# Kernel optimization log

Hardware: AMD Instinct MI355X
Metric: run time of the kernel (lower is better)

## Reference

```python
import jax, jax.numpy as jnp
import numpy as np

AH, AW, TD = 7, 7, 4
SPATIAL_SCALE = 0.0625
TEMP_SCALE = 1.0


def setup_inputs() -> dict:
    key = jax.random.key(0)
    ks = jax.random.split(key, 8)
    N, C, T, H, W = 2, 256, 16, 64, 64
    R = 1024
    features = jax.random.normal(ks[0], (N, C, T, H, W), dtype=jnp.float32)
    img = W / SPATIAL_SCALE  # 1024 px original image
    b = jax.random.randint(ks[1], (R,), 0, N).astype(jnp.float32)
    x1 = jax.random.uniform(ks[2], (R,), minval=0.0, maxval=img * 0.7)
    y1 = jax.random.uniform(ks[3], (R,), minval=0.0, maxval=img * 0.7)
    x2 = x1 + jax.random.uniform(ks[4], (R,), minval=32.0, maxval=img * 0.3)
    y2 = y1 + jax.random.uniform(ks[5], (R,), minval=32.0, maxval=img * 0.3)
    t1 = jax.random.uniform(ks[6], (R,), minval=0.0, maxval=(T - 1) * 0.5)
    t2 = t1 + jax.random.uniform(ks[7], (R,), minval=1.0, maxval=(T - 1) * 0.5)
    rois = jnp.stack([b, x1, y1, t1, x2, y2, t2], axis=1)  # [R,7]
    return {"features": features, "rois": rois}


def _axis_samples(start, end, n, size):
    # legacy roi_align: n grid points spanning the roi, bin = extent/(n-1)
    bin_sz = jnp.maximum(end - start, 0.0) / (n - 1)
    c = start[:, None] + bin_sz[:, None] * jnp.arange(n, dtype=start.dtype)  # [R,n]
    lo = jnp.clip(jnp.floor(c), 0, size - 2).astype(jnp.int32)
    return lo, c - lo, (c >= 0) & (c < size)


def _roi_align_avg(features, rois):
    N, C, T, H, W = features.shape
    Tg, Hg, Wg = TD + 1, AH + 1, AW + 1  # sample on a +1 grid, then avg-pool back
    b = rois[:, 0].astype(jnp.int32)
    t0, ft, vt = _axis_samples(rois[:, 3] * TEMP_SCALE, rois[:, 6] * TEMP_SCALE, Tg, T)
    h0, fh, vh = _axis_samples(rois[:, 2] * SPATIAL_SCALE, rois[:, 5] * SPATIAL_SCALE, Hg, H)
    w0, fw, vw = _axis_samples(rois[:, 1] * SPATIAL_SCALE, rois[:, 4] * SPATIAL_SCALE, Wg, W)
    fm = jnp.transpose(features, (0, 2, 3, 4, 1))  # [N,T,H,W,C] channel-last gather
    b4 = b[:, None, None, None]
    R = rois.shape[0]
    out = jnp.zeros((R, Tg, Hg, Wg, C), dtype=features.dtype)
    for dt in (0, 1):  # 8-corner trilinear interpolation
        wt = ft if dt else (1.0 - ft)
        for dh in (0, 1):
            wh = fh if dh else (1.0 - fh)
            for dw in (0, 1):
                ww = fw if dw else (1.0 - fw)
                corner = fm[b4,
                            (t0 + dt)[:, :, None, None],
                            (h0 + dh)[:, None, :, None],
                            (w0 + dw)[:, None, None, :]]  # [R,Tg,Hg,Wg,C]
                w8 = wt[:, :, None, None] * wh[:, None, :, None] * ww[:, None, None, :]
                out = out + w8[..., None] * corner
    valid = vt[:, :, None, None] & vh[:, None, :, None] & vw[:, None, None, :]
    out = out * valid[..., None].astype(out.dtype)  # samples outside feature map -> 0

    def pool_pairs(a, axis):
        # adaptive_avg_pool from K+1 -> K == kernel-2 stride-1 average
        n = a.shape[axis]
        return 0.5 * (jax.lax.slice_in_dim(a, 0, n - 1, axis=axis)
                      + jax.lax.slice_in_dim(a, 1, n, axis=axis))

    out = pool_pairs(pool_pairs(pool_pairs(out, 1), 2), 3)  # [R,TD,AH,AW,C]
    return jnp.transpose(out, (0, 4, 1, 2, 3))  # [R,C,TD,AH,AW]


def reference(features, rois):
    return _roi_align_avg(features, rois)
```

## Files before the change

### kernel.cpp

```cpp
#include <hip/hip_runtime.h>

#define C_CH 256
#define T_SZ 16
#define H_SZ 64
#define W_SZ 64
#define TGN 5
#define CH 8
#define HWs (H_SZ * W_SZ)
#define CSTR (T_SZ * HWs)
#define NOUT 196
#define KMAX 10

__device__ __forceinline__ float2 ld2a(const float* p) {
    const float2* q = (const float2*)__builtin_assume_aligned(p, 8);
    return *q;
}

__global__ __launch_bounds__(256, 8) void roialign3d_kernel(
    const float* __restrict__ features,
    const float* __restrict__ rois,
    float* __restrict__ out)
{
    const int bid   = blockIdx.x;
    const int sr    = bid >> 13;
    const int rem   = bid & 8191;
    const int r     = rem >> 3;
    const int chunk = (sr << 3) | (rem & 7);
    const int c0    = chunk * CH;

    const int tid  = threadIdx.x;
    const int lane = tid & 63;
    const int wid  = __builtin_amdgcn_readfirstlane(tid >> 6);
    const int hg   = lane >> 3;
    const int wg   = lane & 7;

    __shared__ __align__(16) float sB[KMAX][4];
    __shared__ int sU0, sK;

    const float* roi = rois + r * 7;
    const int   b   = __builtin_amdgcn_readfirstlane((int)roi[0]);
    const float rx1 = roi[1], ry1 = roi[2];
    const float rx2 = roi[4], ry2 = roi[5];

    if (tid < KMAX) {
        const float rt1 = roi[3], rt2 = roi[6];
        const float tbin = fmaxf(rt2 - rt1, 0.0f) * 0.25f;
        int t0a[TGN]; float tw0a[TGN], tw1a[TGN];
        #pragma unroll
        for (int i = 0; i < TGN; ++i) {
            float c  = rt1 + tbin * (float)i;
            float lo = fminf(fmaxf(floorf(c), 0.0f), 14.0f);
            float f  = c - lo;
            float v  = (c >= 0.0f && c < 16.0f) ? 0.125f : 0.0f;
            t0a[i]  = (int)lo;
            tw0a[i] = v * (1.0f - f);
            tw1a[i] = v * f;
        }
        const int u0 = t0a[0];
        const int s0 = u0 + tid;
        float av[TGN];
        #pragma unroll
        for (int i = 0; i < TGN; ++i)
            av[i] = (t0a[i] == s0 ? tw0a[i] : 0.0f)
                  + (t0a[i] + 1 == s0 ? tw1a[i] : 0.0f);
        sB[tid][0] = av[0] + av[1];
        sB[tid][1] = av[1] + av[2];
        sB[tid][2] = av[2] + av[3];
        sB[tid][3] = av[3] + av[4];
        if (tid == 0) { sU0 = u0; sK = t0a[TGN - 1] + 2 - u0; }
    }

    const float hs = ry1 * 0.0625f, he = ry2 * 0.0625f;
    const float hbin = fmaxf(he - hs, 0.0f) * (1.0f / 7.0f);
    const float hc  = hs + hbin * (float)hg;
    const float hlo = fminf(fmaxf(floorf(hc), 0.0f), 62.0f);
    const float hf  = hc - hlo;
    const float hv  = (hc >= 0.0f && hc < 64.0f) ? 1.0f : 0.0f;
    const int   h0  = (int)hlo;
    const float hw0 = hv * (1.0f - hf), hw1 = hv * hf;

    const float wss = rx1 * 0.0625f, wee = rx2 * 0.0625f;
    const float wbin = fmaxf(wee - wss, 0.0f) * (1.0f / 7.0f);
    const float wc  = wss + wbin * (float)wg;
    const float wlo = fminf(fmaxf(floorf(wc), 0.0f), 62.0f);
    const float wf  = wc - wlo;
    const float wv  = (wc >= 0.0f && wc < 64.0f) ? 1.0f : 0.0f;
    const int   w0  = (int)wlo;
    const float ww0 = wv * (1.0f - wf), ww1 = wv * wf;

    const float w00 = hw0 * ww0, w01 = hw0 * ww1;
    const float w10 = hw1 * ww0, w11 = hw1 * ww1;
    const int hw_off = h0 * W_SZ + w0;

    __syncthreads();
    const int u0   = __builtin_amdgcn_readfirstlane(sU0);
    const int kcnt = __builtin_amdgcn_readfirstlane(sK);

    const bool active = (hg < 7) && (wg < 7);
    const int  s_hw   = hg * 7 + wg;

    const float* fcA = features
        + ((size_t)b * C_CH + (size_t)(c0 + wid * 2)) * CSTR
        + (size_t)u0 * HWs + hw_off;
    const float* fcB = fcA + CSTR;

    float oA[4] = {0.f, 0.f, 0.f, 0.f};
    float oB[4] = {0.f, 0.f, 0.f, 0.f};

    #pragma unroll
    for (int u = 0; u < KMAX; ++u) {
        if (u < 2 || u < kcnt) {
            const float4 bb = *(const float4*)sB[u];
            const float* pA = fcA + u * HWs;
            const float* pB = fcB + u * HWs;
            float2 rA0 = ld2a(pA);
            float2 rA1 = ld2a(pA + W_SZ);
            float2 rB0 = ld2a(pB);
            float2 rB1 = ld2a(pB + W_SZ);

            const float bilA = rA0.x * w00 + rA0.y * w01 + rA1.x * w10 + rA1.y * w11;
            const float bilB = rB0.x * w00 + rB0.y * w01 + rB1.x * w10 + rB1.y * w11;

            oA[0] += bb.x * bilA; oA[1] += bb.y * bilA;
            oA[2] += bb.z * bilA; oA[3] += bb.w * bilA;
            oB[0] += bb.x * bilB; oB[1] += bb.y * bilB;
            oB[2] += bb.z * bilB; oB[3] += bb.w * bilB;
        }
    }

    float* ob = out + ((size_t)r * C_CH + (size_t)(c0 + wid * 2)) * NOUT;
    #pragma unroll
    for (int td = 0; td < 4; ++td) {
        float o = oA[td];
        o += __shfl_down(o, 1);
        o += __shfl_down(o, 8);
        if (active) __builtin_nontemporal_store(o, &ob[td * 49 + s_hw]);
    }
    ob += NOUT;
    #pragma unroll
    for (int td = 0; td < 4; ++td) {
        float o = oB[td];
        o += __shfl_down(o, 1);
        o += __shfl_down(o, 8);
        if (active) __builtin_nontemporal_store(o, &ob[td * 49 + s_hw]);
    }
}

extern "C" void kernel_launch(void* const* d_in, const int* in_sizes, int n_in,
                              void* d_out, int out_size, void* d_ws, size_t ws_size,
                              hipStream_t stream) {
    const float* features = (const float*)d_in[0];
    const float* rois     = (const float*)d_in[1];
    float* out            = (float*)d_out;

    int R = in_sizes[1] / 7;
    int nblocks = R * (C_CH / CH);
    hipLaunchKernelGGL(roialign3d_kernel, dim3(nblocks), dim3(256), 0, stream,
                       features, rois, out);
}
```

Measured before the change: 129.7 us.

## Add fast path loading float4 row segments covering two width samples per lane

When the ROI's width bin is at most two pixels, each lane now loads one 4-wide row segment from each of two rows. That segment covers both corners of two adjacent width samples, and each wave handles two channels by splitting lanes into halves. The aim is to halve the number of global load instructions, since the narrow bins let neighbouring samples share the same cache lines. Wider ROIs fall back to the original path. This adds a wave-uniform branch, more select logic for per-position weights, and a reshuffled reduction. The float4 loads assume 16-byte alignment that the computed offsets do not guarantee.

```diff
diff --git a/kernel.cpp b/kernel.cpp
--- a/kernel.cpp
+++ b/kernel.cpp
@@ -13,6 +13,10 @@
 
 __device__ __forceinline__ float2 ld2a(const float* p) {
     const float2* q = (const float2*)__builtin_assume_aligned(p, 8);
+    return *q;
+}
+__device__ __forceinline__ float4 ld4a(const float* p) {
+    const float4* q = (const float4*)__builtin_assume_aligned(p, 16);
     return *q;
 }
 
@@ -31,8 +35,6 @@
     const int tid  = threadIdx.x;
     const int lane = tid & 63;
     const int wid  = __builtin_amdgcn_readfirstlane(tid >> 6);
-    const int hg   = lane >> 3;
-    const int wg   = lane & 7;
 
     __shared__ __align__(16) float sB[KMAX][4];
     __shared__ int sU0, sK;
@@ -69,80 +71,166 @@
         sB[tid][3] = av[3] + av[4];
         if (tid == 0) { sU0 = u0; sK = t0a[TGN - 1] + 2 - u0; }
     }
-
-    const float hs = ry1 * 0.0625f, he = ry2 * 0.0625f;
-    const float hbin = fmaxf(he - hs, 0.0f) * (1.0f / 7.0f);
-    const float hc  = hs + hbin * (float)hg;
-    const float hlo = fminf(fmaxf(floorf(hc), 0.0f), 62.0f);
-    const float hf  = hc - hlo;
-    const float hv  = (hc >= 0.0f && hc < 64.0f) ? 1.0f : 0.0f;
-    const int   h0  = (int)hlo;
-    const float hw0 = hv * (1.0f - hf), hw1 = hv * hf;
-
-    const float wss = rx1 * 0.0625f, wee = rx2 * 0.0625f;
-    const float wbin = fmaxf(wee - wss, 0.0f) * (1.0f / 7.0f);
-    const float wc  = wss + wbin * (float)wg;
-    const float wlo = fminf(fmaxf(floorf(wc), 0.0f), 62.0f);
-    const float wf  = wc - wlo;
-    const float wv  = (wc >= 0.0f && wc < 64.0f) ? 1.0f : 0.0f;
-    const int   w0  = (int)wlo;
-    const float ww0 = wv * (1.0f - wf), ww1 = wv * wf;
-
-    const float w00 = hw0 * ww0, w01 = hw0 * ww1;
-    const float w10 = hw1 * ww0, w11 = hw1 * ww1;
-    const int hw_off = h0 * W_SZ + w0;
-
     __syncthreads();
     const int u0   = __builtin_amdgcn_readfirstlane(sU0);
     const int kcnt = __builtin_amdgcn_readfirstlane(sK);
 
-    const bool active = (hg < 7) && (wg < 7);
-    const int  s_hw   = hg * 7 + wg;
-
-    const float* fcA = features
-        + ((size_t)b * C_CH + (size_t)(c0 + wid * 2)) * CSTR
-        + (size_t)u0 * HWs + hw_off;
-    const float* fcB = fcA + CSTR;
-
-    float oA[4] = {0.f, 0.f, 0.f, 0.f};
-    float oB[4] = {0.f, 0.f, 0.f, 0.f};
-
-    #pragma unroll
-    for (int u = 0; u < KMAX; ++u) {
-        if (u < 2 || u < kcnt) {
-            const float4 bb = *(const float4*)sB[u];
-            const float* pA = fcA + u * HWs;
-            const float* pB = fcB + u * HWs;
-            float2 rA0 = ld2a(pA);
-            float2 rA1 = ld2a(pA + W_SZ);
-            float2 rB0 = ld2a(pB);
-            float2 rB1 = ld2a(pB + W_SZ);
-
-            const float bilA = rA0.x * w00 + rA0.y * w01 + rA1.x * w10 + rA1.y * w11;
-            const float bilB = rB0.x * w00 + rB0.y * w01 + rB1.x * w10 + rB1.y * w11;
-
-            oA[0] += bb.x * bilA; oA[1] += bb.y * bilA;
-            oA[2] += bb.z * bilA; oA[3] += bb.w * bilA;
-            oB[0] += bb.x * bilB; oB[1] += bb.y * bilB;
-            oB[2] += bb.z * bilB; oB[3] += bb.w * bilB;
-        }
-    }
-
-    float* ob = out + ((size_t)r * C_CH + (size_t)(c0 + wid * 2)) * NOUT;
-    #pragma unroll
-    for (int td = 0; td < 4; ++td) {
-        float o = oA[td];
-        o += __shfl_down(o, 1);
-        o += __shfl_down(o, 8);
-        if (active) __builtin_nontemporal_store(o, &ob[td * 49 + s_hw]);
-    }
-    ob += NOUT;
-    #pragma unroll
-    for (int td = 0; td < 4; ++td) {
-        float o = oB[td];
-        o += __shfl_down(o, 1);
-        o += __shfl_down(o, 8);
-        if (active) __builtin_nontemporal_store(o, &ob[td * 49 + s_hw]);
+    const float hs   = ry1 * 0.0625f;
+    const float hbin = fmaxf(ry2 * 0.0625f - hs, 0.0f) * (1.0f / 7.0f);
+    const float wss  = rx1 * 0.0625f;
+    const float wbin = fmaxf(rx2 * 0.0625f - wss, 0.0f) * (1.0f / 7.0f);
+
+    const bool use_fast =
+        (bool)__builtin_amdgcn_readfirstlane((int)(wbin <= 2.0f));
+
+    if (use_fast) {
+        const int ch = lane >> 5;
+        const int hg = (lane >> 2) & 7;
+        const int wp = lane & 3;
+        const int wg0 = wp * 2, wg1 = wg0 + 1;
+
+        const float hc  = hs + hbin * (float)hg;
+        const float hlo = fminf(fmaxf(floorf(hc), 0.0f), 62.0f);
+        const float hf  = hc - hlo;
+        const float hv  = (hc >= 0.0f && hc < 64.0f) ? 1.0f : 0.0f;
+        const int   h0  = (int)hlo;
+        const float hw0 = hv * (1.0f - hf), hw1 = hv * hf;
+
+        const float wc0 = wss + wbin * (float)wg0;
+        const float wl0 = fminf(fmaxf(floorf(wc0), 0.0f), 62.0f);
+        const float wf0 = wc0 - wl0;
+        const float wv0 = (wc0 >= 0.0f && wc0 < 64.0f) ? 1.0f : 0.0f;
+        const int   wi0 = (int)wl0;
+        const float A0  = wv0 * (1.0f - wf0), A1 = wv0 * wf0;
+
+        const float wc1 = wss + wbin * (float)wg1;
+        const float wl1 = fminf(fmaxf(floorf(wc1), 0.0f), 62.0f);
+        const float wf1 = wc1 - wl1;
+        const float wv1 = (wc1 >= 0.0f && wc1 < 64.0f) ? 1.0f : 0.0f;
+        const int   wi1 = (int)wl1;
+        const float B0  = wv1 * (1.0f - wf1), B1 = wv1 * wf1;
+
+        const int base = min(wi0, 60);
+        const int p0   = wi0 - base;
+        const int p1   = wi1 - base;
+
+        const float w0v0 = (p0 == 0) ? A0 : 0.0f;
+        const float w0v1 = (p0 == 1) ? A0 : ((p0 == 0) ? A1 : 0.0f);
+        const float w0v2 = (p0 == 2) ? A0 : ((p0 == 1) ? A1 : 0.0f);
+        const float w0v3 = (p0 == 2) ? A1 : 0.0f;
+        const float w1v0 = (p1 == 0) ? B0 : 0.0f;
+        const float w1v1 = (p1 == 1) ? B0 : ((p1 == 0) ? B1 : 0.0f);
+        const float w1v2 = (p1 == 2) ? B0 : ((p1 == 1) ? B1 : 0.0f);
+        const float w1v3 = (p1 == 2) ? B1 : 0.0f;
+
+        const float* fc = features
+            + ((size_t)b * C_CH + (size_t)(c0 + wid * 2 + ch)) * CSTR
+            + (size_t)u0 * HWs + h0 * W_SZ + base;
+
+        float o0[4] = {0.f, 0.f, 0.f, 0.f};
+        float o1[4] = {0.f, 0.f, 0.f, 0.f};
+
+        #pragma unroll
+        for (int u = 0; u < KMAX; ++u) {
+            if (u < 2 || u < kcnt) {
+                const float4 bb = *(const float4*)sB[u];
+                const float* p = fc + u * HWs;
+                float4 fa = ld4a(p);
+                float4 fb = ld4a(p + W_SZ);
+                const float m0 = hw0 * fa.x + hw1 * fb.x;
+                const float m1 = hw0 * fa.y + hw1 * fb.y;
+                const float m2 = hw0 * fa.z + hw1 * fb.z;
+                const float m3 = hw0 * fa.w + hw1 * fb.w;
+                const float bil0 = m0 * w0v0 + m1 * w0v1 + m2 * w0v2 + m3 * w0v3;
+                const float bil1 = m0 * w1v0 + m1 * w1v1 + m2 * w1v2 + m3 * w1v3;
+                o0[0] += bb.x * bil0; o0[1] += bb.y * bil0;
+                o0[2] += bb.z * bil0; o0[3] += bb.w * bil0;
+                o1[0] += bb.x * bil1; o1[1] += bb.y * bil1;
+                o1[2] += bb.z * bil1; o1[3] += bb.w * bil1;
+            }
+        }
+
+        float* ob = out + ((size_t)r * C_CH + (size_t)(c0 + wid * 2 + ch)) * NOUT;
+        const bool hact = (hg < 7);
+        #pragma unroll
+        for (int td = 0; td < 4; ++td) {
+            float e0 = o0[td] + __shfl_down(o0[td], 4);
+            float e1 = o1[td] + __shfl_down(o1[td], 4);
+            float fe = e0 + e1;
+            float fo = e1 + __shfl_down(e0, 1);
+            if (hact) {
+                __builtin_nontemporal_store(fe, &ob[td * 49 + hg * 7 + wg0]);
+                if (wp < 3)
+                    __builtin_nontemporal_store(fo, &ob[td * 49 + hg * 7 + wg1]);
+            }
+        }
+    } else {
+        const int hg = lane >> 3;
+        const int wg = lane & 7;
+
+        const float hc  = hs + hbin * (float)hg;
+        const float hlo = fminf(fmaxf(floorf(hc), 0.0f), 62.0f);
+        const float hf  = hc - hlo;
+        const float hv  = (hc >= 0.0f && hc < 64.0f) ? 1.0f : 0.0f;
+        const int   h0  = (int)hlo;
+        const float hw0 = hv * (1.0f - hf), hw1 = hv * hf;
+
+        const float wc  = wss + wbin * (float)wg;
+        const float wlo = fminf(fmaxf(floorf(wc), 0.0f), 62.0f);
+        const float wf  = wc - wlo;
+        const float wv  = (wc >= 0.0f && wc < 64.0f) ? 1.0f : 0.0f;
+        const int   w0  = (int)wlo;
+        const float ww0 = wv * (1.0f - wf), ww1 = wv * wf;
+
+        const float w00 = hw0 * ww0, w01 = hw0 * ww1;
+        const float w10 = hw1 * ww0, w11 = hw1 * ww1;
+        const int hw_off = h0 * W_SZ + w0;
+
+        const float* fcA = features
+            + ((size_t)b * C_CH + (size_t)(c0 + wid * 2)) * CSTR
+            + (size_t)u0 * HWs + hw_off;
+        const float* fcB = fcA + CSTR;
+
+        float oA[4] = {0.f, 0.f, 0.f, 0.f};
+        float oB[4] = {0.f, 0.f, 0.f, 0.f};
+
+        #pragma unroll
+        for (int u = 0; u < KMAX; ++u) {
+            if (u < 2 || u < kcnt) {
+                const float4 bb = *(const float4*)sB[u];
+                const float* pA = fcA + u * HWs;
+                const float* pB = fcB + u * HWs;
+                float2 rA0 = ld2a(pA);
+                float2 rA1 = ld2a(pA + W_SZ);
+                float2 rB0 = ld2a(pB);
+                float2 rB1 = ld2a(pB + W_SZ);
+                const float bilA = rA0.x * w00 + rA0.y * w01 + rA1.x * w10 + rA1.y * w11;
+                const float bilB = rB0.x * w00 + rB0.y * w01 + rB1.x * w10 + rB1.y * w11;
+                oA[0] += bb.x * bilA; oA[1] += bb.y * bilA;
+                oA[2] += bb.z * bilA; oA[3] += bb.w * bilA;
+                oB[0] += bb.x * bilB; oB[1] += bb.y * bilB;
+                oB[2] += bb.z * bilB; oB[3] += bb.w * bilB;
+            }
+        }
+
+        const bool active = (hg < 7) && (wg < 7);
+        const int  s_hw   = hg * 7 + wg;
+        float* ob = out + ((size_t)r * C_CH + (size_t)(c0 + wid * 2)) * NOUT;
+        #pragma unroll
+        for (int td = 0; td < 4; ++td) {
+            float o = oA[td];
+            o += __shfl_down(o, 1);
+            o += __shfl_down(o, 8);
+            if (active) __builtin_nontemporal_store(o, &ob[td * 49 + s_hw]);
+        }
+        ob += NOUT;
+        #pragma unroll
+        for (int td = 0; td < 4; ++td) {
+            float o = oB[td];
+            o += __shfl_down(o, 1);
+            o += __shfl_down(o, 8);
+            if (active) __builtin_nontemporal_store(o, &ob[td * 49 + s_hw]);
+        }
     }
 }
 
```

After: 142.8 us. +10.0%, slower.
